# Kernel optimization log

Hardware: AMD Instinct MI355X
Metric: run time of the kernel (lower is better)

## Reference

```python
import jax, jax.numpy as jnp
import numpy as np
jax.config.update("jax_enable_x64", True)

B, N, S, H, D = 64, 13, 128, 768, 512
MAX_DEPTH = 8
MAX_SHAPE_IDS = 256  # min(2**13, 256)


def _gelu(x):
    return jax.nn.gelu(x, approximate=False)  # torch nn.GELU default (erf)


def setup_inputs() -> dict:
    key = jax.random.key(0)
    ks = jax.random.split(key, 12)
    # BFS-complete binary tree with 13 nodes: nodes 0..5 internal, 6..12 leaves
    left = np.array([2 * i + 1 if 2 * i + 2 < N else -1 for i in range(N)], dtype=np.int64)
    right = np.array([2 * i + 2 if 2 * i + 2 < N else -1 for i in range(N)], dtype=np.int64)
    depth = np.array([int(np.floor(np.log2(i + 1))) for i in range(N)], dtype=np.int64)
    is_leaf = np.tile((left == -1)[None, :], (B, 1))  # (B, N) bool
    active = np.ones((B, N), dtype=bool)
    leaf_states = jax.random.normal(ks[0], (B, N, S, H), dtype=jnp.float32)
    leaf_masks = jax.random.bernoulli(ks[1], 0.8, (B, N, S))  # bool
    s = 0.02
    params = dict(
        Wl1=jax.random.normal(ks[2], (H, D), dtype=jnp.float32) * s,
        bl1=jnp.zeros((D,), jnp.float32),
        Wl2=jax.random.normal(ks[3], (D, D), dtype=jnp.float32) * s,
        bl2=jnp.zeros((D,), jnp.float32),
        Wm1=jax.random.normal(ks[4], (2 * D, D), dtype=jnp.float32) * s,
        bm1=jnp.zeros((D,), jnp.float32),
        Wm2=jax.random.normal(ks[5], (D, D), dtype=jnp.float32) * s,
        bm2=jnp.zeros((D,), jnp.float32),
        depth_emb=jax.random.normal(ks[6], (MAX_DEPTH, D), dtype=jnp.float32) * s,
        shape_emb=jax.random.normal(ks[7], (MAX_SHAPE_IDS, D), dtype=jnp.float32) * s,
    )
    return dict(is_leaf=is_leaf, active=active, depth=depth, left_child=left,
                right_child=right, leaf_states=leaf_states, leaf_masks=leaf_masks,
                **params)


def reference(is_leaf, active, depth, left_child, right_child, leaf_states, leaf_masks,
              Wl1, bl1, Wl2, bl2, Wm1, bm1, Wm2, bm2, depth_emb, shape_emb):
    is_leaf = jnp.asarray(is_leaf)
    active = jnp.asarray(active)
    # --- leaf pass (vectorized over all nodes) ---
    maskf = leaf_masks[..., None].astype(leaf_states.dtype)          # (B,N,S,1)
    pooled = (leaf_states * maskf).sum(2) / jnp.maximum(maskf.sum(2), 1.0)  # (B,N,H)
    enc = _gelu(pooled @ Wl1 + bl1) @ Wl2 + bl2                       # (B,N,D)
    enc = enc + depth_emb[jnp.asarray(depth)][None, :, :]             # per-node depth embed
    node_repr = enc * is_leaf[..., None].astype(enc.dtype)            # zero non-leaves
    # --- bottom-up merge (small fixed loop over max_nodes, reverse BFS) ---
    lc_np = np.asarray(left_child)
    rc_np = np.asarray(right_child)
    dp_np = np.asarray(depth)
    for i in range(N - 1, -1, -1):
        lc, rc = int(lc_np[i]), int(rc_np[i])
        if lc == -1:
            continue
        is_internal = active[:, i] & ~is_leaf[:, i]                   # (B,)
        cat = jnp.concatenate([node_repr[:, lc], node_repr[:, rc]], axis=-1)  # (B,2D)
        merged = _gelu(cat @ Wm1 + bm1) @ Wm2 + bm2 + depth_emb[int(dp_np[i])]
        # torch code overwrites the whole column with merged*mask iff any internal
        col = jnp.where(jnp.any(is_internal),
                        merged * is_internal[:, None].astype(merged.dtype),
                        node_repr[:, i])
        node_repr = node_repr.at[:, i].set(col)
    # --- topology hash -> shape embedding ---
    pattern = active.astype(jnp.int64) * 2 + is_leaf.astype(jnp.int64)  # (B,N)
    weights = jnp.array([31 ** i for i in range(N)], dtype=jnp.int64)    # fits int64 for N<=13
    hashed = jnp.abs((pattern * weights[None, :]).sum(1)) % MAX_SHAPE_IDS
    return node_repr[:, 0] + shape_emb[hashed]
```

## Files before the change

### kernel.cpp

```cpp
#include <hip/hip_runtime.h>
#include <hip/hip_bf16.h>
#include <math.h>

#define NN 13
#define SS 128
#define HH 768
#define DD 512

typedef __attribute__((ext_vector_type(8))) short bf16x8;
typedef __attribute__((ext_vector_type(4))) float f32x4;

__device__ __forceinline__ float gelu_f(float x) {
    return 0.5f * x * (1.0f + erff(x * 0.7071067811865475f));
}
__device__ __forceinline__ ushort f2b(float v) {
    __hip_bfloat16 h = __float2bfloat16(v);
    return *reinterpret_cast<ushort*>(&h);
}
__device__ __forceinline__ float b2f(ushort u) {
    __hip_bfloat16 h = *reinterpret_cast<__hip_bfloat16*>(&u);
    return __bfloat162float(h);
}

__device__ __forceinline__ int shape_hash(const int* __restrict__ active,
                                          const int* __restrict__ is_leaf, int b) {
    unsigned long long acc = 0ull, w = 1ull;
    for (int i = 0; i < NN; ++i) {
        unsigned long long p = (unsigned long long)(active[b*NN + i] * 2 + is_leaf[b*NN + i]);
        acc += p * w;
        w *= 31ull;
    }
    long long h = (long long)acc;
    if (h < 0) h = -h;
    return (int)(h % 256);
}

__global__ __launch_bounds__(256)
void transpose_weights(const float* __restrict__ Wl1, const float* __restrict__ Wl2,
                       const float* __restrict__ Wm1, const float* __restrict__ Wm2,
                       ushort* __restrict__ Tl1, ushort* __restrict__ Tl2,
                       ushort* __restrict__ Tm1, ushort* __restrict__ Tm2)
{
    int bx = blockIdx.x;
    const float* W; ushort* T; int K, tile;
    if (bx < 384)       { W = Wl1; T = Tl1; K = 768;  tile = bx; }
    else if (bx < 640)  { W = Wl2; T = Tl2; K = 512;  tile = bx - 384; }
    else if (bx < 1152) { W = Wm1; T = Tm1; K = 1024; tile = bx - 640; }
    else                { W = Wm2; T = Tm2; K = 512;  tile = bx - 1152; }
    int tk = tile >> 4, tj = tile & 15;
    __shared__ float lds[32][33];
    int t = threadIdx.x;
    int r = t >> 3, c0 = (t & 7) * 4;
    const float4 v = *(const float4*)(W + (size_t)(tk*32 + r)*DD + tj*32 + c0);
    lds[r][c0+0] = v.x; lds[r][c0+1] = v.y; lds[r][c0+2] = v.z; lds[r][c0+3] = v.w;
    __syncthreads();
    ushort* dst = T + (size_t)(tj*32 + r)*K + tk*32 + c0;
    dst[0] = f2b(lds[c0+0][r]); dst[1] = f2b(lds[c0+1][r]);
    dst[2] = f2b(lds[c0+2][r]); dst[3] = f2b(lds[c0+3][r]);
}

__global__ __launch_bounds__(192)
void pool_partial(const float* __restrict__ ls, const int* __restrict__ masks,
                  const int* __restrict__ is_leaf,
                  float* __restrict__ part, float* __restrict__ cntbuf)
{
    int idx = blockIdx.x;
    int R = idx >> 2, q = idx & 3;
    int n = R >> 6, b = R & 63;
    if (!is_leaf[b*NN + n]) return;
    const float4* src = (const float4*)(ls + (size_t)(b*NN + n) * SS * HH + (size_t)q * 32 * HH);
    const int* mk = masks + (b*NN + n) * SS + q * 32;
    int t = threadIdx.x;

    __shared__ float lsm[32];
    if (t < 32) lsm[t] = (float)mk[t];
    __syncthreads();

    float4 a = {0.f, 0.f, 0.f, 0.f};
    float cnt = 0.f;
    #pragma unroll 16
    for (int s = 0; s < 32; ++s) {
        float m = lsm[s];
        float4 v = src[s * (HH/4) + t];
        a.x += m * v.x; a.y += m * v.y; a.z += m * v.z; a.w += m * v.w;
        cnt += m;
    }
    ((float4*)(part + ((size_t)q * 832 + R) * HH))[t] = a;
    if (t == 0) cntbuf[q * 832 + R] = cnt;
}

__global__ __launch_bounds__(192)
void pool_combine(const float* __restrict__ part, const float* __restrict__ cntbuf,
                  const int* __restrict__ is_leaf, ushort* __restrict__ pooled)
{
    int u = blockIdx.x;
    int n = u >> 6, b = u & 63;
    int t = threadIdx.x;
    ushort4* dst = (ushort4*)(pooled + (size_t)u * HH);
    if (!is_leaf[b*NN + n]) {
        ushort4 z = {0, 0, 0, 0};
        dst[t] = z;
        return;
    }
    float cnt = cntbuf[u] + cntbuf[832+u] + cntbuf[1664+u] + cntbuf[2496+u];
    float inv = 1.f / fmaxf(cnt, 1.f);
    float4 s = {0.f, 0.f, 0.f, 0.f};
    #pragma unroll
    for (int q = 0; q < 4; ++q) {
        float4 v = ((const float4*)(part + ((size_t)q * 832 + u) * HH))[t];
        s.x += v.x; s.y += v.y; s.z += v.z; s.w += v.w;
    }
    ushort4 o = { f2b(s.x*inv), f2b(s.y*inv), f2b(s.z*inv), f2b(s.w*inv) };
    dst[t] = o;
}

enum { LEAF_G1 = 0, LEAF_G2 = 1, MERGE_G1 = 2, MERGE_G2 = 3, FINAL_G2 = 4 };

template<int MODE, int KT>
__global__ __launch_bounds__(256)
void mfma_gemm(const ushort* __restrict__ Asrc, const ushort* __restrict__ WT,
               const float* __restrict__ bias, void* __restrict__ CoutV,
               const int* __restrict__ is_leaf, const int* __restrict__ active,
               const int* __restrict__ depth, const int* __restrict__ left,
               const int* __restrict__ right,
               const float* __restrict__ depth_emb, const float* __restrict__ shape_emb,
               const ushort* __restrict__ noderep,
               int n0, int n1, int n2)
{
    constexpr int NITER = KT / 32;
    __shared__ ushort a_lds[2][64*40];
    __shared__ ushort b_lds[2][64*40];

    const int t = threadIdx.x;
    const int lane = t & 63, wv = t >> 6;
    const int j0 = blockIdx.x * 64;
    const int by = blockIdx.y;
    const int lrow = lane & 15, lhi = lane >> 4;

    int node, lc = 0, rc = 0;
    if (MODE == LEAF_G1 || MODE == LEAF_G2) {
        node = by;
        bool anyleaf = __any(is_leaf[lane*NN + node] != 0);
        if (!anyleaf) {
            if (MODE == LEAF_G2) {
                ushort* dst = (ushort*)CoutV + (size_t)(node*64)*DD;
                #pragma unroll
                for (int c = 0; c < 4; ++c) {
                    int jc = j0 + c*16 + lrow;
                    #pragma unroll
                    for (int reg = 0; reg < 4; ++reg) {
                        int rw = wv*16 + lhi*4 + reg;
                        dst[(size_t)rw*DD + jc] = 0;
                    }
                }
            }
            return;
        }
    } else {
        node = (by == 0) ? n0 : ((by == 1) ? n1 : n2);
        lc = left[node]; rc = right[node];
    }

    const int AK = (MODE == LEAF_G1) ? HH : DD;
    const int rowbase = (MODE == LEAF_G1 || MODE == LEAF_G2) ? node*64
                       : (MODE == MERGE_G1) ? 0 : by*64;

    const int sr = t >> 2, skg = t & 3;
    f32x4 acc[4];
    #pragma unroll
    for (int c = 0; c < 4; ++c) acc[c] = (f32x4){0.f, 0.f, 0.f, 0.f};

    uint4 aReg, bReg;
    auto loadAB = [&](int kt) {
        int k0 = kt*32 + skg*8;
        const ushort* ap;
        if (MODE == MERGE_G1) {
            ap = (k0 < DD) ? noderep + (size_t)(lc*64 + sr)*DD + k0
                           : noderep + (size_t)(rc*64 + sr)*DD + (k0 - DD);
        } else {
            ap = Asrc + (size_t)(rowbase + sr)*AK + k0;
        }
        aReg = *(const uint4*)ap;
        bReg = *(const uint4*)(WT + (size_t)(j0 + sr)*KT + k0);
    };
    auto storeAB = [&](int buf) {
        *(uint4*)&a_lds[buf][sr*40 + skg*8] = aReg;
        *(uint4*)&b_lds[buf][sr*40 + skg*8] = bReg;
    };

    loadAB(0);
    storeAB(0);
    __syncthreads();

    for (int kt = 0; kt < NITER; ++kt) {
        if (kt + 1 < NITER) loadAB(kt + 1);
        const int buf = kt & 1;
        bf16x8 af = *(const bf16x8*)&a_lds[buf][(wv*16 + lrow)*40 + lhi*8];
        #pragma unroll
        for (int c = 0; c < 4; ++c) {
            bf16x8 bfr = *(const bf16x8*)&b_lds[buf][(c*16 + lrow)*40 + lhi*8];
            acc[c] = __builtin_amdgcn_mfma_f32_16x16x32_bf16(af, bfr, acc[c], 0, 0, 0);
        }
        if (kt + 1 < NITER) storeAB(buf ^ 1);
        __syncthreads();
    }

    if (MODE == LEAF_G1) {
        ushort* H = (ushort*)CoutV + (size_t)(node*64)*DD;
        #pragma unroll
        for (int c = 0; c < 4; ++c) {
            int jc = j0 + c*16 + lrow;
            float bj = bias[jc];
            #pragma unroll
            for (int reg = 0; reg < 4; ++reg) {
                int rw = wv*16 + lhi*4 + reg;
                H[(size_t)rw*DD + jc] = f2b(gelu_f(acc[c][reg] + bj));
            }
        }
    } else if (MODE == LEAF_G2) {
        int dp = depth[node];
        const float* de = depth_emb + (size_t)dp*DD;
        bool lf[4];
        #pragma unroll
        for (int reg = 0; reg < 4; ++reg)
            lf[reg] = is_leaf[(wv*16 + lhi*4 + reg)*NN + node] != 0;
        ushort* dst = (ushort*)CoutV + (size_t)(node*64)*DD;
        #pragma unroll
        for (int c = 0; c < 4; ++c) {
            int jc = j0 + c*16 + lrow;
            float bj = bias[jc] + de[jc];
            #pragma unroll
            for (int reg = 0; reg < 4; ++reg) {
                int rw = wv*16 + lhi*4 + reg;
                dst[(size_t)rw*DD + jc] = f2b(lf[reg] ? (acc[c][reg] + bj) : 0.f);
            }
        }
    } else if (MODE == MERGE_G1) {
        ushort* Mh = (ushort*)CoutV + (size_t)(by*64)*DD;
        #pragma unroll
        for (int c = 0; c < 4; ++c) {
            int jc = j0 + c*16 + lrow;
            float bj = bias[jc];
            #pragma unroll
            for (int reg = 0; reg < 4; ++reg) {
                int rw = wv*16 + lhi*4 + reg;
                Mh[(size_t)rw*DD + jc] = f2b(gelu_f(acc[c][reg] + bj));
            }
        }
    } else {
        int dp = depth[node];
        const float* de = depth_emb + (size_t)dp*DD;
        bool anyInt = __any(active[lane*NN + node] && !is_leaf[lane*NN + node]);
        bool iv[4];
        #pragma unroll
        for (int reg = 0; reg < 4; ++reg) {
            int rw = wv*16 + lhi*4 + reg;
            iv[reg] = active[rw*NN + node] && !is_leaf[rw*NN + node];
        }
        if (MODE == MERGE_G2) {
            if (!anyInt) return;
            ushort* dst = (ushort*)CoutV + (size_t)(node*64)*DD;
            #pragma unroll
            for (int c = 0; c < 4; ++c) {
                int jc = j0 + c*16 + lrow;
                float bj = bias[jc] + de[jc];
                #pragma unroll
                for (int reg = 0; reg < 4; ++reg) {
                    int rw = wv*16 + lhi*4 + reg;
                    dst[(size_t)rw*DD + jc] = f2b(iv[reg] ? (acc[c][reg] + bj) : 0.f);
                }
            }
        } else {
            float* out = (float*)CoutV;
            int hh[4];
            #pragma unroll
            for (int reg = 0; reg < 4; ++reg)
                hh[reg] = shape_hash(active, is_leaf, wv*16 + lhi*4 + reg);
            #pragma unroll
            for (int c = 0; c < 4; ++c) {
                int jc = j0 + c*16 + lrow;
                float bj = bias[jc] + de[jc];
                #pragma unroll
                for (int reg = 0; reg < 4; ++reg) {
                    int rw = wv*16 + lhi*4 + reg;
                    float base = anyInt ? (iv[reg] ? (acc[c][reg] + bj) : 0.f)
                                        : b2f(noderep[(size_t)(node*64 + rw)*DD + jc]);
                    out[(size_t)rw*DD + jc] = base + shape_emb[(size_t)hh[reg]*DD + jc];
                }
            }
        }
    }
}

extern "C" void kernel_launch(void* const* d_in, const int* in_sizes, int n_in,
                              void* d_out, int out_size, void* d_ws, size_t ws_size,
                              hipStream_t stream)
{
    const int*   is_leaf     = (const int*)d_in[0];
    const int*   active      = (const int*)d_in[1];
    const int*   depth       = (const int*)d_in[2];
    const int*   left        = (const int*)d_in[3];
    const int*   right       = (const int*)d_in[4];
    const float* leaf_states = (const float*)d_in[5];
    const int*   leaf_masks  = (const int*)d_in[6];
    const float* Wl1 = (const float*)d_in[7];
    const float* bl1 = (const float*)d_in[8];
    const float* Wl2 = (const float*)d_in[9];
    const float* bl2 = (const float*)d_in[10];
    const float* Wm1 = (const float*)d_in[11];
    const float* bm1 = (const float*)d_in[12];
    const float* Wm2 = (const float*)d_in[13];
    const float* bm2 = (const float*)d_in[14];
    const float* depth_emb = (const float*)d_in[15];
    const float* shape_emb = (const float*)d_in[16];
    float* out = (float*)d_out;

    float* part   = (float*)d_ws;
    float* cntbuf = part + 4*832*768;
    ushort* pooled  = (ushort*)(cntbuf + 4*832);
    ushort* hidden  = pooled + 832*768;
    ushort* noderep = hidden + 832*512;
    ushort* mhid    = noderep + 832*512;
    ushort* Tl1 = mhid + 3*64*512;
    ushort* Tl2 = Tl1 + 512*768;
    ushort* Tm1 = Tl2 + 512*512;
    ushort* Tm2 = Tm1 + 512*1024;

    transpose_weights<<<1408, 256, 0, stream>>>(Wl1, Wl2, Wm1, Wm2, Tl1, Tl2, Tm1, Tm2);

    pool_partial<<<832*4, 192, 0, stream>>>(leaf_states, leaf_masks, is_leaf, part, cntbuf);
    pool_combine<<<832, 192, 0, stream>>>(part, cntbuf, is_leaf, pooled);

    mfma_gemm<LEAF_G1, 768><<<dim3(8, 13), 256, 0, stream>>>(
        pooled, Tl1, bl1, hidden, is_leaf, active, depth, left, right,
        depth_emb, shape_emb, noderep, 0, 0, 0);
    mfma_gemm<LEAF_G2, 512><<<dim3(8, 13), 256, 0, stream>>>(
        hidden, Tl2, bl2, noderep, is_leaf, active, depth, left, right,
        depth_emb, shape_emb, noderep, 0, 0, 0);

    mfma_gemm<MERGE_G1, 1024><<<dim3(8, 3), 256, 0, stream>>>(
        nullptr, Tm1, bm1, mhid, is_leaf, active, depth, left, right,
        depth_emb, shape_emb, noderep, 3, 4, 5);
    mfma_gemm<MERGE_G2, 512><<<dim3(8, 3), 256, 0, stream>>>(
        mhid, Tm2, bm2, noderep, is_leaf, active, depth, left, right,
        depth_emb, shape_emb, noderep, 3, 4, 5);

    mfma_gemm<MERGE_G1, 1024><<<dim3(8, 2), 256, 0, stream>>>(
        nullptr, Tm1, bm1, mhid, is_leaf, active, depth, left, right,
        depth_emb, shape_emb, noderep, 1, 2, 0);
    mfma_gemm<MERGE_G2, 512><<<dim3(8, 2), 256, 0, stream>>>(
        mhid, Tm2, bm2, noderep, is_leaf, active, depth, left, right,
        depth_emb, shape_emb, noderep, 1, 2, 0);

    mfma_gemm<MERGE_G1, 1024><<<dim3(8, 1), 256, 0, stream>>>(
        nullptr, Tm1, bm1, mhid, is_leaf, active, depth, left, right,
        depth_emb, shape_emb, noderep, 0, 0, 0);
    mfma_gemm<FINAL_G2, 512><<<dim3(8, 1), 256, 0, stream>>>(
        mhid, Tm2, bm2, out, is_leaf, active, depth, left, right,
        depth_emb, shape_emb, noderep, 0, 0, 0);
}
```

Measured before the change: 121.6 us.

## Load MFMA operands directly from global memory, dropping LDS double buffering

```diff
diff --git a/kernel.cpp b/kernel.cpp
--- a/kernel.cpp
+++ b/kernel.cpp
@@ -128,8 +128,6 @@
                int n0, int n1, int n2)
 {
     constexpr int NITER = KT / 32;
-    __shared__ ushort a_lds[2][64*40];
-    __shared__ ushort b_lds[2][64*40];
 
     const int t = threadIdx.x;
     const int lane = t & 63, wv = t >> 6;
@@ -164,45 +162,43 @@
     const int AK = (MODE == LEAF_G1) ? HH : DD;
     const int rowbase = (MODE == LEAF_G1 || MODE == LEAF_G2) ? node*64
                        : (MODE == MERGE_G1) ? 0 : by*64;
-
-    const int sr = t >> 2, skg = t & 3;
+    const int arow = wv*16 + lrow;
+
+    const ushort* apL;
+    const ushort* apR = nullptr;
+    if (MODE == MERGE_G1) {
+        apL = noderep + (size_t)(lc*64 + arow)*DD + lhi*8;
+        apR = noderep + (size_t)(rc*64 + arow)*DD + lhi*8;
+    } else {
+        apL = Asrc + (size_t)(rowbase + arow)*AK + lhi*8;
+    }
+    const ushort* bp0 = WT + (size_t)(j0 + 0*16 + lrow)*KT + lhi*8;
+    const ushort* bp1 = WT + (size_t)(j0 + 1*16 + lrow)*KT + lhi*8;
+    const ushort* bp2 = WT + (size_t)(j0 + 2*16 + lrow)*KT + lhi*8;
+    const ushort* bp3 = WT + (size_t)(j0 + 3*16 + lrow)*KT + lhi*8;
+
     f32x4 acc[4];
     #pragma unroll
     for (int c = 0; c < 4; ++c) acc[c] = (f32x4){0.f, 0.f, 0.f, 0.f};
 
-    uint4 aReg, bReg;
-    auto loadAB = [&](int kt) {
-        int k0 = kt*32 + skg*8;
-        const ushort* ap;
+    #pragma unroll 4
+    for (int kt = 0; kt < NITER; ++kt) {
+        const int ko = kt*32;
+        bf16x8 af;
         if (MODE == MERGE_G1) {
-            ap = (k0 < DD) ? noderep + (size_t)(lc*64 + sr)*DD + k0
-                           : noderep + (size_t)(rc*64 + sr)*DD + (k0 - DD);
+            af = (ko < DD) ? *(const bf16x8*)(apL + ko)
+                           : *(const bf16x8*)(apR + (ko - DD));
         } else {
-            ap = Asrc + (size_t)(rowbase + sr)*AK + k0;
-        }
-        aReg = *(const uint4*)ap;
-        bReg = *(const uint4*)(WT + (size_t)(j0 + sr)*KT + k0);
-    };
-    auto storeAB = [&](int buf) {
-        *(uint4*)&a_lds[buf][sr*40 + skg*8] = aReg;
-        *(uint4*)&b_lds[buf][sr*40 + skg*8] = bReg;
-    };
-
-    loadAB(0);
-    storeAB(0);
-    __syncthreads();
-
-    for (int kt = 0; kt < NITER; ++kt) {
-        if (kt + 1 < NITER) loadAB(kt + 1);
-        const int buf = kt & 1;
-        bf16x8 af = *(const bf16x8*)&a_lds[buf][(wv*16 + lrow)*40 + lhi*8];
-        #pragma unroll
-        for (int c = 0; c < 4; ++c) {
-            bf16x8 bfr = *(const bf16x8*)&b_lds[buf][(c*16 + lrow)*40 + lhi*8];
-            acc[c] = __builtin_amdgcn_mfma_f32_16x16x32_bf16(af, bfr, acc[c], 0, 0, 0);
-        }
-        if (kt + 1 < NITER) storeAB(buf ^ 1);
-        __syncthreads();
+            af = *(const bf16x8*)(apL + ko);
+        }
+        bf16x8 b0 = *(const bf16x8*)(bp0 + ko);
+        bf16x8 b1 = *(const bf16x8*)(bp1 + ko);
+        bf16x8 b2 = *(const bf16x8*)(bp2 + ko);
+        bf16x8 b3 = *(const bf16x8*)(bp3 + ko);
+        acc[0] = __builtin_amdgcn_mfma_f32_16x16x32_bf16(af, b0, acc[0], 0, 0, 0);
+        acc[1] = __builtin_amdgcn_mfma_f32_16x16x32_bf16(af, b1, acc[1], 0, 0, 0);
+        acc[2] = __builtin_amdgcn_mfma_f32_16x16x32_bf16(af, b2, acc[2], 0, 0, 0);
+        acc[3] = __builtin_amdgcn_mfma_f32_16x16x32_bf16(af, b3, acc[3], 0, 0, 0);
     }
 
     if (MODE == LEAF_G1) {
```

Measured after the change: 172.1 us. 1.42x slower.

## Split-K GEMM across waves with LDS reduction and merge transpose into pool combine

Applied to the files above, without the earlier changes.

```diff
diff --git a/kernel.cpp b/kernel.cpp
--- a/kernel.cpp
+++ b/kernel.cpp
@@ -33,30 +33,6 @@
     long long h = (long long)acc;
     if (h < 0) h = -h;
     return (int)(h % 256);
-}
-
-__global__ __launch_bounds__(256)
-void transpose_weights(const float* __restrict__ Wl1, const float* __restrict__ Wl2,
-                       const float* __restrict__ Wm1, const float* __restrict__ Wm2,
-                       ushort* __restrict__ Tl1, ushort* __restrict__ Tl2,
-                       ushort* __restrict__ Tm1, ushort* __restrict__ Tm2)
-{
-    int bx = blockIdx.x;
-    const float* W; ushort* T; int K, tile;
-    if (bx < 384)       { W = Wl1; T = Tl1; K = 768;  tile = bx; }
-    else if (bx < 640)  { W = Wl2; T = Tl2; K = 512;  tile = bx - 384; }
-    else if (bx < 1152) { W = Wm1; T = Tm1; K = 1024; tile = bx - 640; }
-    else                { W = Wm2; T = Tm2; K = 512;  tile = bx - 1152; }
-    int tk = tile >> 4, tj = tile & 15;
-    __shared__ float lds[32][33];
-    int t = threadIdx.x;
-    int r = t >> 3, c0 = (t & 7) * 4;
-    const float4 v = *(const float4*)(W + (size_t)(tk*32 + r)*DD + tj*32 + c0);
-    lds[r][c0+0] = v.x; lds[r][c0+1] = v.y; lds[r][c0+2] = v.z; lds[r][c0+3] = v.w;
-    __syncthreads();
-    ushort* dst = T + (size_t)(tj*32 + r)*K + tk*32 + c0;
-    dst[0] = f2b(lds[c0+0][r]); dst[1] = f2b(lds[c0+1][r]);
-    dst[2] = f2b(lds[c0+2][r]); dst[3] = f2b(lds[c0+3][r]);
 }
 
 __global__ __launch_bounds__(192)
@@ -89,29 +65,54 @@
     if (t == 0) cntbuf[q * 832 + R] = cnt;
 }
 
-__global__ __launch_bounds__(192)
-void pool_combine(const float* __restrict__ part, const float* __restrict__ cntbuf,
-                  const int* __restrict__ is_leaf, ushort* __restrict__ pooled)
+__global__ __launch_bounds__(256)
+void combine_transpose(const float* __restrict__ part, const float* __restrict__ cntbuf,
+                       const int* __restrict__ is_leaf, ushort* __restrict__ pooled,
+                       const float* __restrict__ Wl1, const float* __restrict__ Wl2,
+                       const float* __restrict__ Wm1, const float* __restrict__ Wm2,
+                       ushort* __restrict__ Tl1, ushort* __restrict__ Tl2,
+                       ushort* __restrict__ Tm1, ushort* __restrict__ Tm2)
 {
-    int u = blockIdx.x;
-    int n = u >> 6, b = u & 63;
+    int bx = blockIdx.x;
+    if (bx < 832) {
+        int u = bx;
+        int n = u >> 6, b = u & 63;
+        int t = threadIdx.x;
+        if (t >= 192) return;
+        ushort4* dst = (ushort4*)(pooled + (size_t)u * HH);
+        if (!is_leaf[b*NN + n]) {
+            ushort4 z = {0, 0, 0, 0};
+            dst[t] = z;
+            return;
+        }
+        float cnt = cntbuf[u] + cntbuf[832+u] + cntbuf[1664+u] + cntbuf[2496+u];
+        float inv = 1.f / fmaxf(cnt, 1.f);
+        float4 s = {0.f, 0.f, 0.f, 0.f};
+        #pragma unroll
+        for (int q = 0; q < 4; ++q) {
+            float4 v = ((const float4*)(part + ((size_t)q * 832 + u) * HH))[t];
+            s.x += v.x; s.y += v.y; s.z += v.z; s.w += v.w;
+        }
+        ushort4 o = { f2b(s.x*inv), f2b(s.y*inv), f2b(s.z*inv), f2b(s.w*inv) };
+        dst[t] = o;
+        return;
+    }
+    int tb = bx - 832;
+    const float* W; ushort* T; int K, tile;
+    if (tb < 384)       { W = Wl1; T = Tl1; K = 768;  tile = tb; }
+    else if (tb < 640)  { W = Wl2; T = Tl2; K = 512;  tile = tb - 384; }
+    else if (tb < 1152) { W = Wm1; T = Tm1; K = 1024; tile = tb - 640; }
+    else                { W = Wm2; T = Tm2; K = 512;  tile = tb - 1152; }
+    int tk = tile >> 4, tj = tile & 15;
+    __shared__ float lds[32][33];
     int t = threadIdx.x;
-    ushort4* dst = (ushort4*)(pooled + (size_t)u * HH);
-    if (!is_leaf[b*NN + n]) {
-        ushort4 z = {0, 0, 0, 0};
-        dst[t] = z;
-        return;
-    }
-    float cnt = cntbuf[u] + cntbuf[832+u] + cntbuf[1664+u] + cntbuf[2496+u];
-    float inv = 1.f / fmaxf(cnt, 1.f);
-    float4 s = {0.f, 0.f, 0.f, 0.f};
-    #pragma unroll
-    for (int q = 0; q < 4; ++q) {
-        float4 v = ((const float4*)(part + ((size_t)q * 832 + u) * HH))[t];
-        s.x += v.x; s.y += v.y; s.z += v.z; s.w += v.w;
-    }
-    ushort4 o = { f2b(s.x*inv), f2b(s.y*inv), f2b(s.z*inv), f2b(s.w*inv) };
-    dst[t] = o;
+    int r = t >> 3, c0 = (t & 7) * 4;
+    const float4 v = *(const float4*)(W + (size_t)(tk*32 + r)*DD + tj*32 + c0);
+    lds[r][c0+0] = v.x; lds[r][c0+1] = v.y; lds[r][c0+2] = v.z; lds[r][c0+3] = v.w;
+    __syncthreads();
+    ushort* dst = T + (size_t)(tj*32 + r)*K + tk*32 + c0;
+    dst[0] = f2b(lds[c0+0][r]); dst[1] = f2b(lds[c0+1][r]);
+    dst[2] = f2b(lds[c0+2][r]); dst[3] = f2b(lds[c0+3][r]);
 }
 
 enum { LEAF_G1 = 0, LEAF_G2 = 1, MERGE_G1 = 2, MERGE_G2 = 3, FINAL_G2 = 4 };
@@ -127,9 +128,12 @@
                const ushort* __restrict__ noderep,
                int n0, int n1, int n2)
 {
-    constexpr int NITER = KT / 32;
-    __shared__ ushort a_lds[2][64*40];
-    __shared__ ushort b_lds[2][64*40];
+    constexpr int NS = KT / 128;
+    __shared__ __align__(16) ushort sAB[2][64*168];
+    ushort* sA = sAB[0];
+    ushort* sB = sAB[1];
+    float* redA = (float*)sAB[0];
+    float* redB = (float*)sAB[1];
 
     const int t = threadIdx.x;
     const int lane = t & 63, wv = t >> 6;
@@ -165,127 +169,220 @@
     const int rowbase = (MODE == LEAF_G1 || MODE == LEAF_G2) ? node*64
                        : (MODE == MERGE_G1) ? 0 : by*64;
 
-    const int sr = t >> 2, skg = t & 3;
-    f32x4 acc[4];
+    int ur[4], ukc[4];
     #pragma unroll
-    for (int c = 0; c < 4; ++c) acc[c] = (f32x4){0.f, 0.f, 0.f, 0.f};
-
-    uint4 aReg, bReg;
-    auto loadAB = [&](int kt) {
-        int k0 = kt*32 + skg*8;
-        const ushort* ap;
-        if (MODE == MERGE_G1) {
-            ap = (k0 < DD) ? noderep + (size_t)(lc*64 + sr)*DD + k0
-                           : noderep + (size_t)(rc*64 + sr)*DD + (k0 - DD);
-        } else {
-            ap = Asrc + (size_t)(rowbase + sr)*AK + k0;
-        }
-        aReg = *(const uint4*)ap;
-        bReg = *(const uint4*)(WT + (size_t)(j0 + sr)*KT + k0);
+    for (int u = 0; u < 4; ++u) {
+        int chunk = u*256 + t;
+        ur[u] = chunk >> 4;
+        ukc[u] = chunk & 15;
+    }
+
+    f32x4 acc[4][4];
+    #pragma unroll
+    for (int r = 0; r < 4; ++r)
+        #pragma unroll
+        for (int c = 0; c < 4; ++c) acc[r][c] = (f32x4){0.f,0.f,0.f,0.f};
+
+    uint4 aR[4], bR[4];
+    auto prefetch = [&](int ss) {
+        #pragma unroll
+        for (int u = 0; u < 4; ++u) {
+            int kg = ss*128 + ukc[u]*8;
+            const ushort* ap;
+            if (MODE == MERGE_G1) {
+                ap = (kg < DD) ? noderep + (size_t)(lc*64 + ur[u])*DD + kg
+                               : noderep + (size_t)(rc*64 + ur[u])*DD + (kg - DD);
+            } else {
+                ap = Asrc + (size_t)(rowbase + ur[u])*AK + kg;
+            }
+            aR[u] = *(const uint4*)ap;
+            bR[u] = *(const uint4*)(WT + (size_t)(j0 + ur[u])*KT + kg);
+        }
     };
-    auto storeAB = [&](int buf) {
-        *(uint4*)&a_lds[buf][sr*40 + skg*8] = aReg;
-        *(uint4*)&b_lds[buf][sr*40 + skg*8] = bReg;
+    auto commit = [&]() {
+        #pragma unroll
+        for (int u = 0; u < 4; ++u) {
+            int off = ur[u]*168 + (ukc[u] >> 2)*40 + (ukc[u] & 3)*8;
+            *(uint4*)&sA[off] = aR[u];
+            *(uint4*)&sB[off] = bR[u];
+        }
     };
 
-    loadAB(0);
-    storeAB(0);
-    __syncthreads();
-
-    for (int kt = 0; kt < NITER; ++kt) {
-        if (kt + 1 < NITER) loadAB(kt + 1);
-        const int buf = kt & 1;
-        bf16x8 af = *(const bf16x8*)&a_lds[buf][(wv*16 + lrow)*40 + lhi*8];
-        #pragma unroll
-        for (int c = 0; c < 4; ++c) {
-            bf16x8 bfr = *(const bf16x8*)&b_lds[buf][(c*16 + lrow)*40 + lhi*8];
-            acc[c] = __builtin_amdgcn_mfma_f32_16x16x32_bf16(af, bfr, acc[c], 0, 0, 0);
-        }
-        if (kt + 1 < NITER) storeAB(buf ^ 1);
+    prefetch(0);
+    for (int ss = 0; ss < NS; ++ss) {
         __syncthreads();
+        commit();
+        __syncthreads();
+        if (ss + 1 < NS) prefetch(ss + 1);
+        bf16x8 af[4], bf[4];
+        #pragma unroll
+        for (int r = 0; r < 4; ++r)
+            af[r] = *(const bf16x8*)&sA[(r*16 + lrow)*168 + wv*40 + lhi*8];
+        #pragma unroll
+        for (int c = 0; c < 4; ++c)
+            bf[c] = *(const bf16x8*)&sB[(c*16 + lrow)*168 + wv*40 + lhi*8];
+        #pragma unroll
+        for (int r = 0; r < 4; ++r)
+            #pragma unroll
+            for (int c = 0; c < 4; ++c)
+                acc[r][c] = __builtin_amdgcn_mfma_f32_16x16x32_bf16(af[r], bf[c], acc[r][c], 0, 0, 0);
+    }
+
+    auto stf = [&](float* buf, int r, int c, f32x4 v) {
+        *(f32x4*)&buf[((r*4 + c)*64 + lane)*4] = v;
+    };
+    auto ldf = [&](float* buf, int r, int c) {
+        return *(const f32x4*)&buf[((r*4 + c)*64 + lane)*4];
+    };
+    __syncthreads();
+    if (wv == 2) {
+        #pragma unroll
+        for (int r = 0; r < 4; ++r)
+            #pragma unroll
+            for (int c = 0; c < 4; ++c) stf(redA, r, c, acc[r][c]);
+    } else if (wv == 3) {
+        #pragma unroll
+        for (int r = 0; r < 4; ++r)
+            #pragma unroll
+            for (int c = 0; c < 4; ++c) stf(redB, r, c, acc[r][c]);
+    }
+    __syncthreads();
+    if (wv == 0) {
+        #pragma unroll
+        for (int r = 0; r < 4; ++r)
+            #pragma unroll
+            for (int c = 0; c < 4; ++c) { f32x4 v = ldf(redA, r, c); acc[r][c] += v; }
+    } else if (wv == 1) {
+        #pragma unroll
+        for (int r = 0; r < 4; ++r)
+            #pragma unroll
+            for (int c = 0; c < 4; ++c) { f32x4 v = ldf(redB, r, c); acc[r][c] += v; }
+    }
+    __syncthreads();
+    if (wv == 1) {
+        #pragma unroll
+        for (int r = 0; r < 2; ++r)
+            #pragma unroll
+            for (int c = 0; c < 4; ++c) stf(redA, r, c, acc[r][c]);
+    } else if (wv == 0) {
+        #pragma unroll
+        for (int r = 2; r < 4; ++r)
+            #pragma unroll
+            for (int c = 0; c < 4; ++c) stf(redB, r, c, acc[r][c]);
+    }
+    __syncthreads();
+    if (wv >= 2) return;
+    const int rs = wv * 2;
+    if (wv == 0) {
+        #pragma unroll
+        for (int r = 0; r < 2; ++r)
+            #pragma unroll
+            for (int c = 0; c < 4; ++c) { f32x4 v = ldf(redA, r, c); acc[r][c] += v; }
+    } else {
+        #pragma unroll
+        for (int r = 2; r < 4; ++r)
+            #pragma unroll
+            for (int c = 0; c < 4; ++c) { f32x4 v = ldf(redB, r, c); acc[r][c] += v; }
     }
 
     if (MODE == LEAF_G1) {
         ushort* H = (ushort*)CoutV + (size_t)(node*64)*DD;
         #pragma unroll
-        for (int c = 0; c < 4; ++c) {
-            int jc = j0 + c*16 + lrow;
-            float bj = bias[jc];
-            #pragma unroll
-            for (int reg = 0; reg < 4; ++reg) {
-                int rw = wv*16 + lhi*4 + reg;
-                H[(size_t)rw*DD + jc] = f2b(gelu_f(acc[c][reg] + bj));
-            }
-        }
+        for (int rf = 0; rf < 2; ++rf)
+            #pragma unroll
+            for (int c = 0; c < 4; ++c) {
+                int jc = j0 + c*16 + lrow;
+                float bj = bias[jc];
+                #pragma unroll
+                for (int reg = 0; reg < 4; ++reg) {
+                    int rw = (rs+rf)*16 + lhi*4 + reg;
+                    H[(size_t)rw*DD + jc] = f2b(gelu_f(acc[rs+rf][c][reg] + bj));
+                }
+            }
     } else if (MODE == LEAF_G2) {
         int dp = depth[node];
         const float* de = depth_emb + (size_t)dp*DD;
-        bool lf[4];
-        #pragma unroll
-        for (int reg = 0; reg < 4; ++reg)
-            lf[reg] = is_leaf[(wv*16 + lhi*4 + reg)*NN + node] != 0;
         ushort* dst = (ushort*)CoutV + (size_t)(node*64)*DD;
         #pragma unroll
-        for (int c = 0; c < 4; ++c) {
-            int jc = j0 + c*16 + lrow;
-            float bj = bias[jc] + de[jc];
-            #pragma unroll
-            for (int reg = 0; reg < 4; ++reg) {
-                int rw = wv*16 + lhi*4 + reg;
-                dst[(size_t)rw*DD + jc] = f2b(lf[reg] ? (acc[c][reg] + bj) : 0.f);
+        for (int rf = 0; rf < 2; ++rf) {
+            bool lf[4];
+            #pragma unroll
+            for (int reg = 0; reg < 4; ++reg)
+                lf[reg] = is_leaf[((rs+rf)*16 + lhi*4 + reg)*NN + node] != 0;
+            #pragma unroll
+            for (int c = 0; c < 4; ++c) {
+                int jc = j0 + c*16 + lrow;
+                float bj = bias[jc] + de[jc];
+                #pragma unroll
+                for (int reg = 0; reg < 4; ++reg) {
+                    int rw = (rs+rf)*16 + lhi*4 + reg;
+                    dst[(size_t)rw*DD + jc] = f2b(lf[reg] ? (acc[rs+rf][c][reg] + bj) : 0.f);
+                }
             }
         }
     } else if (MODE == MERGE_G1) {
         ushort* Mh = (ushort*)CoutV + (size_t)(by*64)*DD;
         #pragma unroll
-        for (int c = 0; c < 4; ++c) {
-            int jc = j0 + c*16 + lrow;
-            float bj = bias[jc];
-            #pragma unroll
-            for (int reg = 0; reg < 4; ++reg) {
-                int rw = wv*16 + lhi*4 + reg;
-                Mh[(size_t)rw*DD + jc] = f2b(gelu_f(acc[c][reg] + bj));
-            }
-        }
+        for (int rf = 0; rf < 2; ++rf)
+            #pragma unroll
+            for (int c = 0; c < 4; ++c) {
+                int jc = j0 + c*16 + lrow;
+                float bj = bias[jc];
+                #pragma unroll
+                for (int reg = 0; reg < 4; ++reg) {
+                    int rw = (rs+rf)*16 + lhi*4 + reg;
+                    Mh[(size_t)rw*DD + jc] = f2b(gelu_f(acc[rs+rf][c][reg] + bj));
+                }
+            }
     } else {
         int dp = depth[node];
         const float* de = depth_emb + (size_t)dp*DD;
         bool anyInt = __any(active[lane*NN + node] && !is_leaf[lane*NN + node]);
-        bool iv[4];
-        #pragma unroll
-        for (int reg = 0; reg < 4; ++reg) {
-            int rw = wv*16 + lhi*4 + reg;
-            iv[reg] = active[rw*NN + node] && !is_leaf[rw*NN + node];
-        }
         if (MODE == MERGE_G2) {
             if (!anyInt) return;
             ushort* dst = (ushort*)CoutV + (size_t)(node*64)*DD;
             #pragma unroll
-            for (int c = 0; c < 4; ++c) {
-                int jc = j0 + c*16 + lrow;
-                float bj = bias[jc] + de[jc];
+            for (int rf = 0; rf < 2; ++rf) {
+                bool iv[4];
                 #pragma unroll
                 for (int reg = 0; reg < 4; ++reg) {
-                    int rw = wv*16 + lhi*4 + reg;
-                    dst[(size_t)rw*DD + jc] = f2b(iv[reg] ? (acc[c][reg] + bj) : 0.f);
+                    int rw = (rs+rf)*16 + lhi*4 + reg;
+                    iv[reg] = active[rw*NN + node] && !is_leaf[rw*NN + node];
+                }
+                #pragma unroll
+                for (int c = 0; c < 4; ++c) {
+                    int jc = j0 + c*16 + lrow;
+                    float bj = bias[jc] + de[jc];
+                    #pragma unroll
+                    for (int reg = 0; reg < 4; ++reg) {
+                        int rw = (rs+rf)*16 + lhi*4 + reg;
+                        dst[(size_t)rw*DD + jc] = f2b(iv[reg] ? (acc[rs+rf][c][reg] + bj) : 0.f);
+                    }
                 }
             }
         } else {
             float* out = (float*)CoutV;
-            int hh[4];
-            #pragma unroll
-            for (int reg = 0; reg < 4; ++reg)
-                hh[reg] = shape_hash(active, is_leaf, wv*16 + lhi*4 + reg);
-            #pragma unroll
-            for (int c = 0; c < 4; ++c) {
-                int jc = j0 + c*16 + lrow;
-                float bj = bias[jc] + de[jc];
+            #pragma unroll
+            for (int rf = 0; rf < 2; ++rf) {
+                bool iv[4];
+                int hh[4];
                 #pragma unroll
                 for (int reg = 0; reg < 4; ++reg) {
-                    int rw = wv*16 + lhi*4 + reg;
-                    float base = anyInt ? (iv[reg] ? (acc[c][reg] + bj) : 0.f)
-                                        : b2f(noderep[(size_t)(node*64 + rw)*DD + jc]);
-                    out[(size_t)rw*DD + jc] = base + shape_emb[(size_t)hh[reg]*DD + jc];
+                    int rw = (rs+rf)*16 + lhi*4 + reg;
+                    iv[reg] = active[rw*NN + node] && !is_leaf[rw*NN + node];
+                    hh[reg] = shape_hash(active, is_leaf, rw);
+                }
+                #pragma unroll
+                for (int c = 0; c < 4; ++c) {
+                    int jc = j0 + c*16 + lrow;
+                    float bj = bias[jc] + de[jc];
+                    #pragma unroll
+                    for (int reg = 0; reg < 4; ++reg) {
+                        int rw = (rs+rf)*16 + lhi*4 + reg;
+                        float base = anyInt ? (iv[reg] ? (acc[rs+rf][c][reg] + bj) : 0.f)
+                                            : b2f(noderep[(size_t)(node*64 + rw)*DD + jc]);
+                        out[(size_t)rw*DD + jc] = base + shape_emb[(size_t)hh[reg]*DD + jc];
+                    }
                 }
             }
         }
@@ -326,10 +423,9 @@
     ushort* Tm1 = Tl2 + 512*512;
     ushort* Tm2 = Tm1 + 512*1024;
 
-    transpose_weights<<<1408, 256, 0, stream>>>(Wl1, Wl2, Wm1, Wm2, Tl1, Tl2, Tm1, Tm2);
-
     pool_partial<<<832*4, 192, 0, stream>>>(leaf_states, leaf_masks, is_leaf, part, cntbuf);
-    pool_combine<<<832, 192, 0, stream>>>(part, cntbuf, is_leaf, pooled);
+    combine_transpose<<<832 + 1408, 256, 0, stream>>>(part, cntbuf, is_leaf, pooled,
+                                                      Wl1, Wl2, Wm1, Wm2, Tl1, Tl2, Tm1, Tm2);
 
     mfma_gemm<LEAF_G1, 768><<<dim3(8, 13), 256, 0, stream>>>(
         pooled, Tl1, bl1, hidden, is_leaf, active, depth, left, right,
```

New measurement: 312.2 us. 157% more time.

## Merge weight transpose into pool combine and double K-step per GEMM stage

Applied to the files above, without the earlier changes.

```diff
diff --git a/kernel.cpp b/kernel.cpp
--- a/kernel.cpp
+++ b/kernel.cpp
@@ -33,30 +33,6 @@
     long long h = (long long)acc;
     if (h < 0) h = -h;
     return (int)(h % 256);
-}
-
-__global__ __launch_bounds__(256)
-void transpose_weights(const float* __restrict__ Wl1, const float* __restrict__ Wl2,
-                       const float* __restrict__ Wm1, const float* __restrict__ Wm2,
-                       ushort* __restrict__ Tl1, ushort* __restrict__ Tl2,
-                       ushort* __restrict__ Tm1, ushort* __restrict__ Tm2)
-{
-    int bx = blockIdx.x;
-    const float* W; ushort* T; int K, tile;
-    if (bx < 384)       { W = Wl1; T = Tl1; K = 768;  tile = bx; }
-    else if (bx < 640)  { W = Wl2; T = Tl2; K = 512;  tile = bx - 384; }
-    else if (bx < 1152) { W = Wm1; T = Tm1; K = 1024; tile = bx - 640; }
-    else                { W = Wm2; T = Tm2; K = 512;  tile = bx - 1152; }
-    int tk = tile >> 4, tj = tile & 15;
-    __shared__ float lds[32][33];
-    int t = threadIdx.x;
-    int r = t >> 3, c0 = (t & 7) * 4;
-    const float4 v = *(const float4*)(W + (size_t)(tk*32 + r)*DD + tj*32 + c0);
-    lds[r][c0+0] = v.x; lds[r][c0+1] = v.y; lds[r][c0+2] = v.z; lds[r][c0+3] = v.w;
-    __syncthreads();
-    ushort* dst = T + (size_t)(tj*32 + r)*K + tk*32 + c0;
-    dst[0] = f2b(lds[c0+0][r]); dst[1] = f2b(lds[c0+1][r]);
-    dst[2] = f2b(lds[c0+2][r]); dst[3] = f2b(lds[c0+3][r]);
 }
 
 __global__ __launch_bounds__(192)
@@ -89,29 +65,54 @@
     if (t == 0) cntbuf[q * 832 + R] = cnt;
 }
 
-__global__ __launch_bounds__(192)
-void pool_combine(const float* __restrict__ part, const float* __restrict__ cntbuf,
-                  const int* __restrict__ is_leaf, ushort* __restrict__ pooled)
+__global__ __launch_bounds__(256)
+void combine_transpose(const float* __restrict__ part, const float* __restrict__ cntbuf,
+                       const int* __restrict__ is_leaf, ushort* __restrict__ pooled,
+                       const float* __restrict__ Wl1, const float* __restrict__ Wl2,
+                       const float* __restrict__ Wm1, const float* __restrict__ Wm2,
+                       ushort* __restrict__ Tl1, ushort* __restrict__ Tl2,
+                       ushort* __restrict__ Tm1, ushort* __restrict__ Tm2)
 {
-    int u = blockIdx.x;
-    int n = u >> 6, b = u & 63;
+    int bx = blockIdx.x;
+    if (bx < 832) {
+        int u = bx;
+        int n = u >> 6, b = u & 63;
+        int t = threadIdx.x;
+        if (t >= 192) return;
+        ushort4* dst = (ushort4*)(pooled + (size_t)u * HH);
+        if (!is_leaf[b*NN + n]) {
+            ushort4 z = {0, 0, 0, 0};
+            dst[t] = z;
+            return;
+        }
+        float cnt = cntbuf[u] + cntbuf[832+u] + cntbuf[1664+u] + cntbuf[2496+u];
+        float inv = 1.f / fmaxf(cnt, 1.f);
+        float4 s = {0.f, 0.f, 0.f, 0.f};
+        #pragma unroll
+        for (int q = 0; q < 4; ++q) {
+            float4 v = ((const float4*)(part + ((size_t)q * 832 + u) * HH))[t];
+            s.x += v.x; s.y += v.y; s.z += v.z; s.w += v.w;
+        }
+        ushort4 o = { f2b(s.x*inv), f2b(s.y*inv), f2b(s.z*inv), f2b(s.w*inv) };
+        dst[t] = o;
+        return;
+    }
+    int tb = bx - 832;
+    const float* W; ushort* T; int K, tile;
+    if (tb < 384)       { W = Wl1; T = Tl1; K = 768;  tile = tb; }
+    else if (tb < 640)  { W = Wl2; T = Tl2; K = 512;  tile = tb - 384; }
+    else if (tb < 1152) { W = Wm1; T = Tm1; K = 1024; tile = tb - 640; }
+    else                { W = Wm2; T = Tm2; K = 512;  tile = tb - 1152; }
+    int tk = tile >> 4, tj = tile & 15;
+    __shared__ float lds[32][33];
     int t = threadIdx.x;
-    ushort4* dst = (ushort4*)(pooled + (size_t)u * HH);
-    if (!is_leaf[b*NN + n]) {
-        ushort4 z = {0, 0, 0, 0};
-        dst[t] = z;
-        return;
-    }
-    float cnt = cntbuf[u] + cntbuf[832+u] + cntbuf[1664+u] + cntbuf[2496+u];
-    float inv = 1.f / fmaxf(cnt, 1.f);
-    float4 s = {0.f, 0.f, 0.f, 0.f};
-    #pragma unroll
-    for (int q = 0; q < 4; ++q) {
-        float4 v = ((const float4*)(part + ((size_t)q * 832 + u) * HH))[t];
-        s.x += v.x; s.y += v.y; s.z += v.z; s.w += v.w;
-    }
-    ushort4 o = { f2b(s.x*inv), f2b(s.y*inv), f2b(s.z*inv), f2b(s.w*inv) };
-    dst[t] = o;
+    int r = t >> 3, c0 = (t & 7) * 4;
+    const float4 v = *(const float4*)(W + (size_t)(tk*32 + r)*DD + tj*32 + c0);
+    lds[r][c0+0] = v.x; lds[r][c0+1] = v.y; lds[r][c0+2] = v.z; lds[r][c0+3] = v.w;
+    __syncthreads();
+    ushort* dst = T + (size_t)(tj*32 + r)*K + tk*32 + c0;
+    dst[0] = f2b(lds[c0+0][r]); dst[1] = f2b(lds[c0+1][r]);
+    dst[2] = f2b(lds[c0+2][r]); dst[3] = f2b(lds[c0+3][r]);
 }
 
 enum { LEAF_G1 = 0, LEAF_G2 = 1, MERGE_G1 = 2, MERGE_G2 = 3, FINAL_G2 = 4 };
@@ -127,9 +128,9 @@
                const ushort* __restrict__ noderep,
                int n0, int n1, int n2)
 {
-    constexpr int NITER = KT / 32;
-    __shared__ ushort a_lds[2][64*40];
-    __shared__ ushort b_lds[2][64*40];
+    constexpr int NS = KT / 64;
+    __shared__ ushort a_lds[2][2][64*40];
+    __shared__ ushort b_lds[2][2][64*40];
 
     const int t = threadIdx.x;
     const int lane = t & 63, wv = t >> 6;
@@ -170,38 +171,47 @@
     #pragma unroll
     for (int c = 0; c < 4; ++c) acc[c] = (f32x4){0.f, 0.f, 0.f, 0.f};
 
-    uint4 aReg, bReg;
-    auto loadAB = [&](int kt) {
-        int k0 = kt*32 + skg*8;
-        const ushort* ap;
-        if (MODE == MERGE_G1) {
-            ap = (k0 < DD) ? noderep + (size_t)(lc*64 + sr)*DD + k0
-                           : noderep + (size_t)(rc*64 + sr)*DD + (k0 - DD);
-        } else {
-            ap = Asrc + (size_t)(rowbase + sr)*AK + k0;
-        }
-        aReg = *(const uint4*)ap;
-        bReg = *(const uint4*)(WT + (size_t)(j0 + sr)*KT + k0);
+    uint4 aReg[2], bReg[2];
+    auto loadAB = [&](int ss) {
+        #pragma unroll
+        for (int ch = 0; ch < 2; ++ch) {
+            int k0 = ss*64 + ch*32 + skg*8;
+            const ushort* ap;
+            if (MODE == MERGE_G1) {
+                ap = (k0 < DD) ? noderep + (size_t)(lc*64 + sr)*DD + k0
+                               : noderep + (size_t)(rc*64 + sr)*DD + (k0 - DD);
+            } else {
+                ap = Asrc + (size_t)(rowbase + sr)*AK + k0;
+            }
+            aReg[ch] = *(const uint4*)ap;
+            bReg[ch] = *(const uint4*)(WT + (size_t)(j0 + sr)*KT + k0);
+        }
     };
     auto storeAB = [&](int buf) {
-        *(uint4*)&a_lds[buf][sr*40 + skg*8] = aReg;
-        *(uint4*)&b_lds[buf][sr*40 + skg*8] = bReg;
+        #pragma unroll
+        for (int ch = 0; ch < 2; ++ch) {
+            *(uint4*)&a_lds[buf][ch][sr*40 + skg*8] = aReg[ch];
+            *(uint4*)&b_lds[buf][ch][sr*40 + skg*8] = bReg[ch];
+        }
     };
 
     loadAB(0);
     storeAB(0);
     __syncthreads();
 
-    for (int kt = 0; kt < NITER; ++kt) {
-        if (kt + 1 < NITER) loadAB(kt + 1);
-        const int buf = kt & 1;
-        bf16x8 af = *(const bf16x8*)&a_lds[buf][(wv*16 + lrow)*40 + lhi*8];
-        #pragma unroll
-        for (int c = 0; c < 4; ++c) {
-            bf16x8 bfr = *(const bf16x8*)&b_lds[buf][(c*16 + lrow)*40 + lhi*8];
-            acc[c] = __builtin_amdgcn_mfma_f32_16x16x32_bf16(af, bfr, acc[c], 0, 0, 0);
-        }
-        if (kt + 1 < NITER) storeAB(buf ^ 1);
+    for (int ss = 0; ss < NS; ++ss) {
+        if (ss + 1 < NS) loadAB(ss + 1);
+        const int buf = ss & 1;
+        #pragma unroll
+        for (int ch = 0; ch < 2; ++ch) {
+            bf16x8 af = *(const bf16x8*)&a_lds[buf][ch][(wv*16 + lrow)*40 + lhi*8];
+            #pragma unroll
+            for (int c = 0; c < 4; ++c) {
+                bf16x8 bfr = *(const bf16x8*)&b_lds[buf][ch][(c*16 + lrow)*40 + lhi*8];
+                acc[c] = __builtin_amdgcn_mfma_f32_16x16x32_bf16(af, bfr, acc[c], 0, 0, 0);
+            }
+        }
+        if (ss + 1 < NS) storeAB(buf ^ 1);
         __syncthreads();
     }
 
@@ -326,10 +336,9 @@
     ushort* Tm1 = Tl2 + 512*512;
     ushort* Tm2 = Tm1 + 512*1024;
 
-    transpose_weights<<<1408, 256, 0, stream>>>(Wl1, Wl2, Wm1, Wm2, Tl1, Tl2, Tm1, Tm2);
-
     pool_partial<<<832*4, 192, 0, stream>>>(leaf_states, leaf_masks, is_leaf, part, cntbuf);
-    pool_combine<<<832, 192, 0, stream>>>(part, cntbuf, is_leaf, pooled);
+    combine_transpose<<<832 + 1408, 256, 0, stream>>>(part, cntbuf, is_leaf, pooled,
+                                                      Wl1, Wl2, Wm1, Wm2, Tl1, Tl2, Tm1, Tm2);
 
     mfma_gemm<LEAF_G1, 768><<<dim3(8, 13), 256, 0, stream>>>(
         pooled, Tl1, bl1, hidden, is_leaf, active, depth, left, right,
```

Result: slower. 184.2 us (+51.5%).
